# Performance work log

Measured on AMD Instinct MI355X. Metric: run time of the kernel, lower is better.

## Reference

```python
import jax, jax.numpy as jnp
import numpy as np

N_NODES = 100000
N_EDGES = 1280000
IN_C = 64
HID_C = 64
OUT_C = 64


def _sage_conv(x, src, dst, W_l, b_l, W_r, num_nodes):
    """PyG SAGEConv with mean aggregation:
    out = lin_l(mean_{j in N(i)} x_j) + lin_r(x_i)
    lin_l has bias, lin_r (root) has no bias."""
    msg = x[src]  # [E, C] gather of source-node features
    summed = jax.ops.segment_sum(msg, dst, num_segments=num_nodes)  # [N, C]
    cnt = jax.ops.segment_sum(jnp.ones((src.shape[0], 1), x.dtype), dst,
                              num_segments=num_nodes)  # [N, 1]
    agg = summed / jnp.maximum(cnt, 1)  # mean; isolated nodes -> 0
    return agg @ W_l.T + b_l + x @ W_r.T


def setup_inputs() -> dict:
    key = jax.random.key(0)
    ks = jax.random.split(key, 8)
    x = jax.random.normal(ks[0], (N_NODES, IN_C), dtype=jnp.float32)
    edge_index = jax.random.randint(ks[1], (2, N_EDGES), 0, N_NODES, dtype=jnp.int64)
    s1 = 1.0 / np.sqrt(IN_C)
    s2 = 1.0 / np.sqrt(HID_C)
    W1_l = jax.random.uniform(ks[2], (HID_C, IN_C), jnp.float32, -s1, s1)
    b1 = jax.random.uniform(ks[3], (HID_C,), jnp.float32, -s1, s1)
    W1_r = jax.random.uniform(ks[4], (HID_C, IN_C), jnp.float32, -s1, s1)
    W2_l = jax.random.uniform(ks[5], (OUT_C, HID_C), jnp.float32, -s2, s2)
    b2 = jax.random.uniform(ks[6], (OUT_C,), jnp.float32, -s2, s2)
    W2_r = jax.random.uniform(ks[7], (OUT_C, HID_C), jnp.float32, -s2, s2)
    return {"x": x, "edge_index": edge_index, "W1_l": W1_l, "b1": b1,
            "W1_r": W1_r, "W2_l": W2_l, "b2": b2, "W2_r": W2_r}


def reference(x, edge_index, W1_l, b1, W1_r, W2_l, b2, W2_r):
    src, dst = edge_index[0], edge_index[1]
    h = _sage_conv(x, src, dst, W1_l, b1, W1_r, N_NODES)
    h = jax.nn.relu(h)
    out = _sage_conv(h, src, dst, W2_l, b2, W2_r, N_NODES)
    return out
```

## Files before the change

### kernel.cpp

```cpp
#include <hip/hip_runtime.h>

constexpr int N = 100000;
constexpr int E = 1280000;
constexpr int C = 64;
constexpr int NB = (N + 255) / 256;
constexpr int EPB = 4096;
constexpr int NBIN = (E + EPB - 1) / EPB;
constexpr int EPB2 = 8192;
constexpr int NBIN2 = (E + EPB2 - 1) / EPB2;
constexpr int CAP = 4096;

typedef __attribute__((ext_vector_type(8))) short bf16x8;
typedef __attribute__((ext_vector_type(4))) float f32x4;

__device__ __forceinline__ unsigned bfr(float v) {
    unsigned u = __float_as_uint(v);
    return (u + 0x7fffu + ((u >> 16) & 1u)) >> 16;
}
__device__ __forceinline__ float bflo(unsigned w) { return __uint_as_float(w << 16); }
__device__ __forceinline__ float bfhi(unsigned w) { return __uint_as_float(w & 0xffff0000u); }

constexpr int CASTB = (N * 16 + 255) / 256;
constexpr int WCB = 8;
__global__ __launch_bounds__(256) void prep_k(
    const float* __restrict__ x, uint2* __restrict__ xb,
    const float* __restrict__ W1l, const float* __restrict__ W1r, unsigned* __restrict__ Wb1,
    const float* __restrict__ W2l, const float* __restrict__ W2r, unsigned* __restrict__ Wb2,
    const int* __restrict__ dst, int* __restrict__ bcnt) {
    int blk = blockIdx.x;
    int t = threadIdx.x;
    if (blk < CASTB) {
        int i = blk * 256 + t;
        if (i < N * 16) {
            float4 v = ((const float4*)x)[i];
            uint2 o;
            o.x = bfr(v.x) | (bfr(v.y) << 16);
            o.y = bfr(v.z) | (bfr(v.w) << 16);
            xb[i] = o;
        }
        return;
    }
    if (blk < CASTB + 2 * WCB) {
        int wb = blk - CASTB;
        const float* Wl = (wb < WCB) ? W1l : W2l;
        const float* Wr = (wb < WCB) ? W1r : W2r;
        unsigned* Wb = (wb < WCB) ? Wb1 : Wb2;
        int u = ((wb < WCB) ? wb : wb - WCB) * 256 + t;
        int c = u >> 5;
        int p = u & 31;
        float2 l = *(const float2*)(Wl + c * 64 + p * 2);
        float2 r = *(const float2*)(Wr + c * 64 + p * 2);
        Wb[c * 64 + p]      = bfr(l.x) | (bfr(l.y) << 16);
        Wb[c * 64 + 32 + p] = bfr(r.x) | (bfr(r.y) << 16);
        return;
    }
    __shared__ int h[NB];
    int cb = blk - CASTB - 2 * WCB;
    for (int i = t; i < NB; i += 256) h[i] = 0;
    __syncthreads();
    int e0 = cb * EPB;
    int eEnd = min(e0 + EPB, E);
    for (int e = e0 + t; e < eEnd; e += 256) atomicAdd(&h[dst[e] >> 8], 1);
    __syncthreads();
    for (int i = t; i < NB; i += 256)
        if (h[i]) atomicAdd(&bcnt[i], h[i]);
}

__global__ __launch_bounds__(512) void scanB_k(const int* __restrict__ bcnt,
                                               int* __restrict__ bbase,
                                               int* __restrict__ gcur) {
    __shared__ int s[2][512];
    int t = threadIdx.x;
    int v = (t < NB) ? bcnt[t] : 0;
    s[0][t] = v;
    __syncthreads();
    int p = 0;
    for (int off = 1; off < 512; off <<= 1) {
        int a = s[p][t] + (t >= off ? s[p][t - off] : 0);
        s[p ^ 1][t] = a;
        p ^= 1;
        __syncthreads();
    }
    if (t < NB) { bbase[t] = s[p][t] - v; gcur[t] = 0; }
}

__global__ __launch_bounds__(512) void bin_k(const int* __restrict__ src,
                                             const int* __restrict__ dst,
                                             const int* __restrict__ bbase,
                                             int* __restrict__ gcur,
                                             unsigned* __restrict__ tmp) {
    __shared__ int hist[NB];
    __shared__ int start[NB];
    __shared__ int cnt2[NB];
    __shared__ int gbase[NB];
    __shared__ unsigned pk[EPB2];
    __shared__ unsigned short bkt[EPB2];
    __shared__ int sc[2][512];
    int t = threadIdx.x;
    for (int i = t; i < NB; i += 512) { hist[i] = 0; cnt2[i] = 0; }
    __syncthreads();
    int e0 = blockIdx.x * EPB2;
    int eEnd = min(e0 + EPB2, E);
    for (int e = e0 + t; e < eEnd; e += 512) atomicAdd(&hist[dst[e] >> 8], 1);
    __syncthreads();
    int v = (t < NB) ? hist[t] : 0;
    sc[0][t] = v;
    __syncthreads();
    int p = 0;
    for (int off = 1; off < 512; off <<= 1) {
        int a = sc[p][t] + (t >= off ? sc[p][t - off] : 0);
        sc[p ^ 1][t] = a;
        p ^= 1;
        __syncthreads();
    }
    if (t < NB) start[t] = sc[p][t] - v;
    __syncthreads();
    for (int e = e0 + t; e < eEnd; e += 512) {
        int d = dst[e];
        int b = d >> 8;
        int pos = start[b] + atomicAdd(&cnt2[b], 1);
        pk[pos] = ((unsigned)src[e] << 8) | (unsigned)(d & 255);
        bkt[pos] = (unsigned short)b;
    }
    __syncthreads();
    for (int i = t; i < NB; i += 512)
        gbase[i] = hist[i] ? bbase[i] + atomicAdd(&gcur[i], hist[i]) : 0;
    __syncthreads();
    int n = eEnd - e0;
    for (int i = t; i < n; i += 512) {
        int b = bkt[i];
        tmp[gbase[b] + (i - start[b])] = pk[i];
    }
}

__global__ __launch_bounds__(512) void bsort_k(const unsigned* __restrict__ tmp,
                                               const int* __restrict__ bbase,
                                               const int* __restrict__ bcnt,
                                               int* __restrict__ rowp,
                                               int* __restrict__ deg,
                                               int* __restrict__ csr) {
    int b = blockIdx.x;
    int base = bbase[b];
    int count = bcnt[b];
    __shared__ int h[256], st[256], c2[256];
    __shared__ int sc[2][256];
    __shared__ unsigned srcA[CAP];
    int t = threadIdx.x;
    if (t < 256) { h[t] = 0; c2[t] = 0; }
    __syncthreads();
    for (int i = t; i < count; i += 512) atomicAdd(&h[tmp[base + i] & 255u], 1);
    __syncthreads();
    if (t < 256) sc[0][t] = h[t];
    __syncthreads();
    int p = 0;
    for (int off = 1; off < 256; off <<= 1) {
        if (t < 256) sc[p ^ 1][t] = sc[p][t] + (t >= off ? sc[p][t - off] : 0);
        p ^= 1;
        __syncthreads();
    }
    if (t < 256) {
        int excl = sc[p][t] - h[t];
        st[t] = excl;
        int node = b * 256 + t;
        if (node < N) { rowp[node] = base + excl; deg[node] = h[t]; }
    }
    __syncthreads();
    for (int i = t; i < count; i += 512) {
        unsigned pr = tmp[base + i];
        int d = (int)(pr & 255u);
        int pos = st[d] + atomicAdd(&c2[d], 1);
        srcA[pos] = pr >> 8;
    }
    __syncthreads();
    for (int i = t; i < count; i += 512) csr[base + i] = (int)srcA[i];
}

__global__ __launch_bounds__(256) void agg_k(const int* __restrict__ csr,
                                             const int* __restrict__ rowp,
                                             const int* __restrict__ deg,
                                             const uint2* __restrict__ featb,
                                             uint2* __restrict__ aggb) {
    int node = blockIdx.x * 4 + (threadIdx.x >> 6);
    int lane = threadIdx.x & 63;
    int g = lane >> 4;
    int q = lane & 15;
    int start = rowp[node];
    int d = deg[node];
    float4 acc = make_float4(0.f, 0.f, 0.f, 0.f);
    int j = g;
    for (; j + 4 < d; j += 8) {
        int s0 = csr[start + j];
        int s1 = csr[start + j + 4];
        uint2 u0 = featb[(size_t)s0 * 16 + q];
        uint2 u1 = featb[(size_t)s1 * 16 + q];
        acc.x += bflo(u0.x) + bflo(u1.x);
        acc.y += bfhi(u0.x) + bfhi(u1.x);
        acc.z += bflo(u0.y) + bflo(u1.y);
        acc.w += bfhi(u0.y) + bfhi(u1.y);
    }
    for (; j < d; j += 4) {
        int s0 = csr[start + j];
        uint2 u0 = featb[(size_t)s0 * 16 + q];
        acc.x += bflo(u0.x); acc.y += bfhi(u0.x);
        acc.z += bflo(u0.y); acc.w += bfhi(u0.y);
    }
#pragma unroll
    for (int off = 16; off <= 32; off <<= 1) {
        acc.x += __shfl_xor(acc.x, off);
        acc.y += __shfl_xor(acc.y, off);
        acc.z += __shfl_xor(acc.z, off);
        acc.w += __shfl_xor(acc.w, off);
    }
    if (g == 0) {
        float inv = d > 0 ? 1.f / (float)d : 0.f;
        uint2 o;
        o.x = bfr(acc.x * inv) | (bfr(acc.y * inv) << 16);
        o.y = bfr(acc.z * inv) | (bfr(acc.w * inv) << 16);
        aggb[(size_t)node * 16 + q] = o;
    }
}

template <int RELU, int OBF>
__global__ __launch_bounds__(256) void combine_mfma_k(
    const unsigned short* __restrict__ Ab,
    const unsigned short* __restrict__ Xb,
    const unsigned short* __restrict__ Wb,
    const float* __restrict__ bias,
    float* __restrict__ outF, unsigned short* __restrict__ outB) {
    int wave = threadIdx.x >> 6;
    int lane = threadIdx.x & 63;
    int row0 = (blockIdx.x * 4 + wave) * 16;
    if (row0 >= N) return;
    int g = lane >> 4;
    int r = lane & 15;
    int node = row0 + r;

    const unsigned short* arow = Ab + (size_t)node * 64 + g * 8;
    const unsigned short* xrow = Xb + (size_t)node * 64 + g * 8;
    bf16x8 a[4];
    a[0] = *(const bf16x8*)(const void*)(arow);
    a[1] = *(const bf16x8*)(const void*)(arow + 32);
    a[2] = *(const bf16x8*)(const void*)(xrow);
    a[3] = *(const bf16x8*)(const void*)(xrow + 32);

#pragma unroll
    for (int ct = 0; ct < 4; ++ct) {
        int c = ct * 16 + r;
        const unsigned short* wrow = Wb + (size_t)c * 128 + g * 8;
        f32x4 acc = {0.f, 0.f, 0.f, 0.f};
#pragma unroll
        for (int kc = 0; kc < 4; ++kc) {
            bf16x8 b = *(const bf16x8*)(const void*)(wrow + kc * 32);
            acc = __builtin_amdgcn_mfma_f32_16x16x32_bf16(a[kc], b, acc, 0, 0, 0);
        }
        float bs = bias[c];
#pragma unroll
        for (int rr = 0; rr < 4; ++rr) {
            int orow = row0 + g * 4 + rr;
            float v = acc[rr] + bs;
            if (RELU) v = fmaxf(v, 0.f);
            if (OBF) {
                float v1 = __shfl_xor(v, 1);
                if ((lane & 1) == 0) {
                    unsigned u = bfr(v) | (bfr(v1) << 16);
                    *(unsigned*)(void*)(outB + (size_t)orow * 64 + c) = u;
                }
            } else {
                outF[(size_t)orow * 64 + c] = v;
            }
        }
    }
}

extern "C" void kernel_launch(void* const* d_in, const int* in_sizes, int n_in,
                              void* d_out, int out_size, void* d_ws, size_t ws_size,
                              hipStream_t stream) {
    const float* x   = (const float*)d_in[0];
    const int*   ei  = (const int*)d_in[1];
    const int*   srcI = ei;
    const int*   dstI = ei + E;
    const float* W1l = (const float*)d_in[2];
    const float* b1  = (const float*)d_in[3];
    const float* W1r = (const float*)d_in[4];
    const float* W2l = (const float*)d_in[5];
    const float* b2  = (const float*)d_in[6];
    const float* W2r = (const float*)d_in[7];
    float* out = (float*)d_out;

    int*            bcnt  = (int*)d_ws;
    int*            bbase = bcnt + 512;
    int*            gcur  = bbase + 512;
    int*            deg   = gcur + 512;
    int*            rowp  = deg + 102400;
    int*            csr   = rowp + 102400;
    unsigned short* aggb  = (unsigned short*)(csr + E);
    unsigned short* xb    = aggb + (size_t)N * 64;
    unsigned short* hb    = xb + (size_t)N * 64;
    unsigned*       Wb1   = (unsigned*)(hb + (size_t)N * 64);
    unsigned*       Wb2   = Wb1 + 64 * 64;
    unsigned*       tmp   = (unsigned*)aggb;

    hipMemsetAsync(bcnt, 0, 512 * sizeof(int), stream);

    prep_k<<<CASTB + 2 * WCB + NBIN, 256, 0, stream>>>(
        x, (uint2*)xb, W1l, W1r, Wb1, W2l, W2r, Wb2, dstI, bcnt);
    scanB_k<<<1, 512, 0, stream>>>(bcnt, bbase, gcur);
    bin_k<<<NBIN2, 512, 0, stream>>>(srcI, dstI, bbase, gcur, tmp);
    bsort_k<<<NB, 512, 0, stream>>>(tmp, bbase, bcnt, rowp, deg, csr);

    const int nAggBlocks = N / 4;
    const int nMfmaBlocks = (N / 16 + 3) / 4;

    agg_k<<<nAggBlocks, 256, 0, stream>>>(csr, rowp, deg, (const uint2*)xb, (uint2*)aggb);
    combine_mfma_k<1, 1><<<nMfmaBlocks, 256, 0, stream>>>(
        aggb, xb, (const unsigned short*)Wb1, b1, nullptr, hb);

    agg_k<<<nAggBlocks, 256, 0, stream>>>(csr, rowp, deg, (const uint2*)hb, (uint2*)aggb);
    combine_mfma_k<0, 0><<<nMfmaBlocks, 256, 0, stream>>>(
        aggb, hb, (const unsigned short*)Wb2, b2, out, nullptr);
}
```

Baseline: 168.9 us.

## Fuse neighbor aggregation and MFMA combine into one kernel per layer

Merges the mean-aggregation kernel and the MFMA linear-combine kernel into a single kernel per SAGE layer. Each 256-thread block aggregates 16 nodes into shared memory, then each wave computes one 16-column output tile with MFMA. This removes the global round trip of the aggregated buffer and two kernel launches. The cost is a block-wide barrier and fewer nodes in flight per wave during the latency-bound gather. The temporary bin buffer is moved to its own workspace region because the aggregation buffer it used to share no longer exists.

```diff
diff --git a/kernel.cpp b/kernel.cpp
--- a/kernel.cpp
+++ b/kernel.cpp
@@ -175,99 +175,92 @@
     for (int i = t; i < count; i += 512) csr[base + i] = (int)srcA[i];
 }
 
-__global__ __launch_bounds__(256) void agg_k(const int* __restrict__ csr,
-                                             const int* __restrict__ rowp,
-                                             const int* __restrict__ deg,
-                                             const uint2* __restrict__ featb,
-                                             uint2* __restrict__ aggb) {
-    int node = blockIdx.x * 4 + (threadIdx.x >> 6);
+template <int RELU, int OBF>
+__global__ __launch_bounds__(256) void aggcomb_k(
+    const int* __restrict__ csr, const int* __restrict__ rowp,
+    const int* __restrict__ deg,
+    const unsigned short* __restrict__ Fb,
+    const unsigned short* __restrict__ Wb,
+    const float* __restrict__ bias,
+    float* __restrict__ outF, unsigned short* __restrict__ outB) {
+    __shared__ unsigned short sAgg[16][72];
+    const uint2* featb = (const uint2*)Fb;
+    int tile = blockIdx.x * 16;
+    int w = threadIdx.x >> 6;
     int lane = threadIdx.x & 63;
     int g = lane >> 4;
     int q = lane & 15;
-    int start = rowp[node];
-    int d = deg[node];
-    float4 acc = make_float4(0.f, 0.f, 0.f, 0.f);
-    int j = g;
-    for (; j + 4 < d; j += 8) {
-        int s0 = csr[start + j];
-        int s1 = csr[start + j + 4];
-        uint2 u0 = featb[(size_t)s0 * 16 + q];
-        uint2 u1 = featb[(size_t)s1 * 16 + q];
-        acc.x += bflo(u0.x) + bflo(u1.x);
-        acc.y += bfhi(u0.x) + bfhi(u1.x);
-        acc.z += bflo(u0.y) + bflo(u1.y);
-        acc.w += bfhi(u0.y) + bfhi(u1.y);
-    }
-    for (; j < d; j += 4) {
-        int s0 = csr[start + j];
-        uint2 u0 = featb[(size_t)s0 * 16 + q];
-        acc.x += bflo(u0.x); acc.y += bfhi(u0.x);
-        acc.z += bflo(u0.y); acc.w += bfhi(u0.y);
-    }
+
+    for (int s = 0; s < 4; ++s) {
+        int node = tile + w * 4 + s;
+        int start = rowp[node];
+        int d = deg[node];
+        float4 acc = make_float4(0.f, 0.f, 0.f, 0.f);
+        int j = g;
+        for (; j + 4 < d; j += 8) {
+            int s0 = csr[start + j];
+            int s1 = csr[start + j + 4];
+            uint2 u0 = featb[(size_t)s0 * 16 + q];
+            uint2 u1 = featb[(size_t)s1 * 16 + q];
+            acc.x += bflo(u0.x) + bflo(u1.x);
+            acc.y += bfhi(u0.x) + bfhi(u1.x);
+            acc.z += bflo(u0.y) + bflo(u1.y);
+            acc.w += bfhi(u0.y) + bfhi(u1.y);
+        }
+        for (; j < d; j += 4) {
+            int s0 = csr[start + j];
+            uint2 u0 = featb[(size_t)s0 * 16 + q];
+            acc.x += bflo(u0.x); acc.y += bfhi(u0.x);
+            acc.z += bflo(u0.y); acc.w += bfhi(u0.y);
+        }
 #pragma unroll
-    for (int off = 16; off <= 32; off <<= 1) {
-        acc.x += __shfl_xor(acc.x, off);
-        acc.y += __shfl_xor(acc.y, off);
-        acc.z += __shfl_xor(acc.z, off);
-        acc.w += __shfl_xor(acc.w, off);
-    }
-    if (g == 0) {
-        float inv = d > 0 ? 1.f / (float)d : 0.f;
-        uint2 o;
-        o.x = bfr(acc.x * inv) | (bfr(acc.y * inv) << 16);
-        o.y = bfr(acc.z * inv) | (bfr(acc.w * inv) << 16);
-        aggb[(size_t)node * 16 + q] = o;
-    }
-}
-
-template <int RELU, int OBF>
-__global__ __launch_bounds__(256) void combine_mfma_k(
-    const unsigned short* __restrict__ Ab,
-    const unsigned short* __restrict__ Xb,
-    const unsigned short* __restrict__ Wb,
-    const float* __restrict__ bias,
-    float* __restrict__ outF, unsigned short* __restrict__ outB) {
-    int wave = threadIdx.x >> 6;
-    int lane = threadIdx.x & 63;
-    int row0 = (blockIdx.x * 4 + wave) * 16;
-    if (row0 >= N) return;
-    int g = lane >> 4;
-    int r = lane & 15;
-    int node = row0 + r;
-
-    const unsigned short* arow = Ab + (size_t)node * 64 + g * 8;
-    const unsigned short* xrow = Xb + (size_t)node * 64 + g * 8;
+        for (int off = 16; off <= 32; off <<= 1) {
+            acc.x += __shfl_xor(acc.x, off);
+            acc.y += __shfl_xor(acc.y, off);
+            acc.z += __shfl_xor(acc.z, off);
+            acc.w += __shfl_xor(acc.w, off);
+        }
+        if (g == 0) {
+            float inv = d > 0 ? 1.f / (float)d : 0.f;
+            uint2 o;
+            o.x = bfr(acc.x * inv) | (bfr(acc.y * inv) << 16);
+            o.y = bfr(acc.z * inv) | (bfr(acc.w * inv) << 16);
+            *(uint2*)&sAgg[w * 4 + s][q * 4] = o;
+        }
+    }
+    __syncthreads();
+
+    int r = q;
+    int node = tile + r;
+    const unsigned short* xrow = Fb + (size_t)node * 64 + g * 8;
     bf16x8 a[4];
-    a[0] = *(const bf16x8*)(const void*)(arow);
-    a[1] = *(const bf16x8*)(const void*)(arow + 32);
+    a[0] = *(const bf16x8*)(const void*)&sAgg[r][g * 8];
+    a[1] = *(const bf16x8*)(const void*)&sAgg[r][32 + g * 8];
     a[2] = *(const bf16x8*)(const void*)(xrow);
     a[3] = *(const bf16x8*)(const void*)(xrow + 32);
 
+    int c = w * 16 + r;
+    const unsigned short* wrow = Wb + (size_t)c * 128 + g * 8;
+    f32x4 acc = {0.f, 0.f, 0.f, 0.f};
 #pragma unroll
-    for (int ct = 0; ct < 4; ++ct) {
-        int c = ct * 16 + r;
-        const unsigned short* wrow = Wb + (size_t)c * 128 + g * 8;
-        f32x4 acc = {0.f, 0.f, 0.f, 0.f};
+    for (int kc = 0; kc < 4; ++kc) {
+        bf16x8 b = *(const bf16x8*)(const void*)(wrow + kc * 32);
+        acc = __builtin_amdgcn_mfma_f32_16x16x32_bf16(a[kc], b, acc, 0, 0, 0);
+    }
+    float bs = bias[c];
 #pragma unroll
-        for (int kc = 0; kc < 4; ++kc) {
-            bf16x8 b = *(const bf16x8*)(const void*)(wrow + kc * 32);
-            acc = __builtin_amdgcn_mfma_f32_16x16x32_bf16(a[kc], b, acc, 0, 0, 0);
-        }
-        float bs = bias[c];
-#pragma unroll
-        for (int rr = 0; rr < 4; ++rr) {
-            int orow = row0 + g * 4 + rr;
-            float v = acc[rr] + bs;
-            if (RELU) v = fmaxf(v, 0.f);
-            if (OBF) {
-                float v1 = __shfl_xor(v, 1);
-                if ((lane & 1) == 0) {
-                    unsigned u = bfr(v) | (bfr(v1) << 16);
-                    *(unsigned*)(void*)(outB + (size_t)orow * 64 + c) = u;
-                }
-            } else {
-                outF[(size_t)orow * 64 + c] = v;
+    for (int rr = 0; rr < 4; ++rr) {
+        int orow = tile + g * 4 + rr;
+        float v = acc[rr] + bs;
+        if (RELU) v = fmaxf(v, 0.f);
+        if (OBF) {
+            float v1 = __shfl_xor(v, 1);
+            if ((lane & 1) == 0) {
+                unsigned u = bfr(v) | (bfr(v1) << 16);
+                *(unsigned*)(void*)(outB + (size_t)orow * 64 + c) = u;
             }
+        } else {
+            outF[(size_t)orow * 64 + c] = v;
         }
     }
 }
@@ -293,12 +286,11 @@
     int*            deg   = gcur + 512;
     int*            rowp  = deg + 102400;
     int*            csr   = rowp + 102400;
-    unsigned short* aggb  = (unsigned short*)(csr + E);
-    unsigned short* xb    = aggb + (size_t)N * 64;
+    unsigned*       tmp   = (unsigned*)(csr + E);
+    unsigned short* xb    = (unsigned short*)(tmp + E);
     unsigned short* hb    = xb + (size_t)N * 64;
     unsigned*       Wb1   = (unsigned*)(hb + (size_t)N * 64);
     unsigned*       Wb2   = Wb1 + 64 * 64;
-    unsigned*       tmp   = (unsigned*)aggb;
 
     hipMemsetAsync(bcnt, 0, 512 * sizeof(int), stream);
 
@@ -308,14 +300,11 @@
     bin_k<<<NBIN2, 512, 0, stream>>>(srcI, dstI, bbase, gcur, tmp);
     bsort_k<<<NB, 512, 0, stream>>>(tmp, bbase, bcnt, rowp, deg, csr);
 
-    const int nAggBlocks = N / 4;
-    const int nMfmaBlocks = (N / 16 + 3) / 4;
-
-    agg_k<<<nAggBlocks, 256, 0, stream>>>(csr, rowp, deg, (const uint2*)xb, (uint2*)aggb);
-    combine_mfma_k<1, 1><<<nMfmaBlocks, 256, 0, stream>>>(
-        aggb, xb, (const unsigned short*)Wb1, b1, nullptr, hb);
-
-    agg_k<<<nAggBlocks, 256, 0, stream>>>(csr, rowp, deg, (const uint2*)hb, (uint2*)aggb);
-    combine_mfma_k<0, 0><<<nMfmaBlocks, 256, 0, stream>>>(
-        aggb, hb, (const unsigned short*)Wb2, b2, out, nullptr);
-}
+    const int nTileBlocks = N / 16;
+
+    aggcomb_k<1, 1><<<nTileBlocks, 256, 0, stream>>>(
+        csr, rowp, deg, xb, (const unsigned short*)Wb1, b1, nullptr, hb);
+
+    aggcomb_k<0, 0><<<nTileBlocks, 256, 0, stream>>>(
+        csr, rowp, deg, hb, (const unsigned short*)Wb2, b2, out, nullptr);
+}
```

Result: faster. 159.6 us (median of 2 runs) (-5.5%).
